# Performance work log

Hardware: AMD Instinct MI355X
Metric: run time of the kernel (lower is better)

The kernel has to match this reference:

```python
import jax, jax.numpy as jnp
import numpy as np

N_TRAIN = 2000
N_ATOMS = 30
DIM_D = N_ATOMS * (N_ATOMS - 1) // 2   # 435 pairwise descriptor entries
DIM_I = 3 * N_ATOMS                    # 90 Cartesian dofs
N_PERMS = 12
SIG = 10.0

_ROWS, _COLS = np.tril_indices(N_ATOMS, -1)
_DR = np.arange(DIM_D)


def d_desc_from_comp(Rd):
    # Rd: [n, DIM_D, 3] compact pair derivatives -> full Jacobian [n, DIM_D, DIM_I]
    # each pair (a,b) contributes +d at atom a's 3 dofs and -d at atom b's.
    n = Rd.shape[0]
    out = jnp.zeros((n, DIM_D, N_ATOMS, 3), Rd.dtype)
    out = out.at[:, _DR, _ROWS, :].set(Rd)
    out = out.at[:, _DR, _COLS, :].set(-Rd)
    return out.reshape(n, DIM_D, DIM_I)


def setup_inputs() -> dict:
    key = jax.random.key(0)
    k1, k2 = jax.random.split(key)
    R_desc = jax.random.normal(k1, (N_TRAIN, DIM_D), jnp.float32)
    R_d_desc = jax.random.normal(k2, (N_TRAIN, DIM_D, 3), jnp.float32)
    # Build a permutation-consistent tril_perms_lin (identity + random atom perms).
    rng = np.random.RandomState(0)
    M = np.zeros((N_ATOMS, N_ATOMS), np.int64)
    M[_ROWS, _COLS] = np.arange(DIM_D)
    M[_COLS, _ROWS] = np.arange(DIM_D)
    tril_perms = np.empty((N_PERMS, DIM_D), np.int64)
    for p in range(N_PERMS):
        perm = np.arange(N_ATOMS) if p == 0 else rng.permutation(N_ATOMS)
        tril_perms[p] = M[perm[_ROWS], perm[_COLS]]
    tpl = (tril_perms + np.arange(N_PERMS)[:, None] * DIM_D).flatten(order='F')
    return {
        'R_desc': R_desc,
        'R_d_desc': R_d_desc,
        'tril_perms_lin': jnp.asarray(tpl),
        'j': 0,
    }


def reference(R_desc, R_d_desc, tril_perms_lin, j):
    q = np.sqrt(5.0) / SIG
    # column point j: expanded Jacobian [DIM_D, DIM_I]
    rj_d = d_desc_from_comp(R_d_desc[j][None])[0]
    # permutation-symmetrized descriptor / Jacobian for point j
    rj_desc_perms = jnp.tile(R_desc[j], N_PERMS)[tril_perms_lin].reshape(DIM_D, N_PERMS).T  # [P,D]
    rj_d_perms = jnp.tile(rj_d.T, (1, N_PERMS))[:, tril_perms_lin].reshape(DIM_I, DIM_D, N_PERMS)  # [3N,D,P]
    x_diffs = q * (R_desc[:, None, :] - rj_desc_perms[None])        # [n,P,D]
    x_dists = jnp.linalg.norm(x_diffs, axis=-1)                      # [n,P]
    exp_xs = jnp.exp(-x_dists) * (q * q / 3.0)                       # [n,P]
    exp_xs_1_x_dists = exp_xs * (1.0 + x_dists)                      # [n,P]
    # Matern-5/2 Hessian block assembly
    inner = jnp.einsum('npd,jdp->npj', x_diffs, rj_d_perms)          # [n,P,3N]
    diff_ab = jnp.einsum('npd,npj->ndj', x_diffs * exp_xs[:, :, None], inner)  # [n,D,3N]
    diff_ab = diff_ab - jnp.einsum('jdp,np->ndj', rj_d_perms, exp_xs_1_x_dists)
    Rd_full = d_desc_from_comp(R_d_desc)                             # [n,D,3N]
    k = jnp.einsum('ndj,ndk->nkj', diff_ab, Rd_full)                 # [n,3N,3N]
    return k.reshape(N_TRAIN * DIM_I, DIM_I)
```

## Files before the change

kernel.cpp:

```cpp
#include <hip/hip_runtime.h>
#include <math.h>

#define NA 30
#define ND 435
#define NI 90
#define NP 12
#define NNB (NA-1)
#define SST 91
#define NTHR 384

typedef float v2f __attribute__((ext_vector_type(2)));

struct Pre {
  int   pidx[NP][ND];
  int   sigma[NP][NA];
  int   sigma_inv[NP][NA];
  int   rowv[ND];
  int   colv[ND];
  float rjp[NP][ND];
  float spj[NA][SST];
  unsigned int gtab[NNB][NP][NA];
  alignas(16) unsigned int stab[NA][NA][NP];
  unsigned int hmask[NA][NA];
};

__device__ __forceinline__ int pair_index(int x, int y) {
  int hi = max(x, y), lo = min(x, y);
  return hi * (hi - 1) / 2 + lo;
}

__global__ void preA_kernel(const int* __restrict__ tpl, Pre* ws) {
  const int tid = threadIdx.x;
  const int nthr = blockDim.x;

  for (int d = tid; d < ND; d += nthr) {
    int a = (int)floorf((1.0f + sqrtf(1.0f + 8.0f * (float)d)) * 0.5f);
    while (a * (a - 1) / 2 > d) --a;
    while ((a + 1) * a / 2 <= d) ++a;
    ws->rowv[d] = a;
    ws->colv[d] = d - a * (a - 1) / 2;
  }
  for (int idx = tid; idx < NP * ND; idx += nthr) {
    int d = idx / NP, p = idx % NP;
    ws->pidx[p][d] = tpl[idx] - p * ND;
  }
  __syncthreads();
  for (int idx = tid; idx < NP * NA; idx += nthr) {
    int p = idx / NA, a = idx % NA;
    int u1 = (a == 0) ? 1 : 0;
    int u2 = (a <= 1) ? 2 : 1;
    int e1 = ws->pidx[p][pair_index(a, u1)];
    int e2 = ws->pidx[p][pair_index(a, u2)];
    int r1 = ws->rowv[e1], c1 = ws->colv[e1];
    int r2 = ws->rowv[e2], c2 = ws->colv[e2];
    int sa = (r1 == r2 || r1 == c2) ? r1 : c1;
    ws->sigma[p][a] = sa;
  }
  __syncthreads();
  for (int idx = tid; idx < NP * NA; idx += nthr) {
    int p = idx / NA, a = idx % NA;
    ws->sigma_inv[p][ws->sigma[p][a]] = a;
  }
  __syncthreads();
  for (int it = tid; it < NA * NA; it += nthr) {
    int a = it / NA, a2 = it % NA;
    unsigned m = 0;
#pragma unroll
    for (int p = 0; p < NP; ++p)
      if (ws->sigma[p][a] == a2) m |= (1u << p);
    ws->hmask[a][a2] = m;
  }
}

__global__ void preB_kernel(const float* __restrict__ R_desc,
                            const float* __restrict__ R_d_desc,
                            const int* __restrict__ jptr,
                            Pre* ws) {
  const int gid = blockIdx.x * blockDim.x + threadIdx.x;
  const int gsz = gridDim.x * blockDim.x;
  const int j = *jptr;

  for (int idx = gid; idx < NP * ND; idx += gsz) {
    int p = idx / ND, d = idx % ND;
    ws->rjp[p][d] = R_desc[(size_t)j * ND + ws->pidx[p][d]];
  }
  for (int idx = gid; idx < NA * SST; idx += gsz) {
    int a = idx / SST, r = idx % SST;
    float val = 0.f;
    if (r < NI) {
      int u = r / 3, c = r % 3;
      if (u != a) {
        int d = pair_index(a, u);
        float t = R_d_desc[(size_t)j * (ND * 3) + 3 * d + c];
        val = (a > u) ? t : -t;
      }
    }
    ((float*)ws->spj)[idx] = val;
  }
  for (int idx = gid; idx < NNB * NP * NA; idx += gsz) {
    int a = idx % NA;
    int r = idx / NA;
    int p = r % NP, k = r / NP;
    int u = k + (k >= a ? 1 : 0);
    int d = pair_index(a, u);
    int su = ws->sigma[p][u];
    ws->gtab[k][p][a] = (unsigned)d | ((unsigned)su << 9) | ((unsigned)u << 14);
  }
  for (int idx = gid; idx < NA * NA * NP; idx += gsz) {
    int p = idx % NP;
    int r = idx / NP;
    int a2 = r % NA, a = r / NA;
    unsigned int v = 0;
    if (ws->sigma[p][a] != a2) {
      int u = ws->sigma_inv[p][a2];
      int sa = ws->sigma[p][a];
      v = (unsigned)u | ((unsigned)sa << 5) | (1u << 15);
    }
    ws->stab[a][a2][p] = v;
  }
}

__global__ __launch_bounds__(NTHR, 4) void gdml_kernel(
    const float* __restrict__ R_desc,
    const float* __restrict__ R_d_desc,
    const Pre* __restrict__ ws,
    float* __restrict__ out) {
  const int n = blockIdx.x;
  const int tid = threadIdx.x;

  __shared__ float rn_l[ND];
  __shared__ float S[NA * SST];
  __shared__ float Sp[NA * SST];
  __shared__ float v_s[NP * NI];
  __shared__ float w_s[NP * NI];
  __shared__ alignas(16) unsigned short HhU[NA * NP * 9];
  __shared__ float dist2[NP];
  __shared__ float e_s[NP], e1_s[NP];

  const float q   = 0.22360679774997896f;
  const float qq3 = 0.016666666666666666f;

  if (tid < NP) dist2[tid] = 0.f;
  for (int d = tid; d < ND; d += NTHR) rn_l[d] = R_desc[(size_t)n * ND + d];
  float* raw = (float*)HhU;
  for (int i = tid; i < ND * 3; i += NTHR)
    raw[i] = R_d_desc[(size_t)n * (ND * 3) + i];
  for (int i = tid; i < NA * SST; i += NTHR)
    Sp[i] = ((const float*)ws->spj)[i];
  __syncthreads();

  for (int i = tid; i < NA * NI; i += NTHR) {
    int a = i / NI, r = i % NI;
    int u = r / 3, c = r % 3;
    float val = 0.f;
    if (u != a) {
      int d = pair_index(a, u);
      float t = raw[3 * d + c];
      val = (a > u) ? t : -t;
    }
    S[a * SST + r] = val;
  }
  __syncthreads();

  float h[9];
  const int a_i = tid % NA, p_i = tid / NA;
  const bool act = (tid < NP * NA);
  if (act) {
    int sa = ws->sigma[p_i][a_i];
    const float* Srow = S + a_i * SST;
    const float* Prow = Sp + sa * SST;
    const float* rjpp = &ws->rjp[p_i][0];
    v2f V01 = {0.f, 0.f}; float V2 = 0.f;
    v2f I01 = {0.f, 0.f}; float I2 = 0.f;
    v2f H0 = {0.f, 0.f}, H1 = {0.f, 0.f}, H2 = {0.f, 0.f};
    float Hc0 = 0.f, Hc1 = 0.f, Hc2 = 0.f;
    float xq = 0.f;
    for (int k = 0; k < NNB; ++k) {
      unsigned g = ws->gtab[k][p_i][a_i];
      int d  = g & 511;
      int su = (g >> 9) & 31;
      int u  = (g >> 14) & 31;
      float x = q * (rn_l[d] - rjpp[d]);
      xq += x * x;
      float s0 = Srow[3 * u], s1 = Srow[3 * u + 1], s2 = Srow[3 * u + 2];
      float t0 = Prow[3 * su], t1 = Prow[3 * su + 1], t2 = Prow[3 * su + 2];
      V01 += (v2f){x, x} * (v2f){s0, s1}; V2 += x * s2;
      I01 += (v2f){x, x} * (v2f){t0, t1}; I2 += x * t2;
      v2f t01 = {t0, t1};
      H0 += (v2f){s0, s0} * t01; Hc0 += s0 * t2;
      H1 += (v2f){s1, s1} * t01; Hc1 += s1 * t2;
      H2 += (v2f){s2, s2} * t01; Hc2 += s2 * t2;
    }
    v_s[p_i * NI + 3 * a_i + 0] = V01.x;
    v_s[p_i * NI + 3 * a_i + 1] = V01.y;
    v_s[p_i * NI + 3 * a_i + 2] = V2;
    w_s[p_i * NI + 3 * sa + 0] = I01.x;
    w_s[p_i * NI + 3 * sa + 1] = I01.y;
    w_s[p_i * NI + 3 * sa + 2] = I2;
    atomicAdd(&dist2[p_i], xq);
    h[0] = H0.x; h[1] = H0.y; h[2] = Hc0;
    h[3] = H1.x; h[4] = H1.y; h[5] = Hc1;
    h[6] = H2.x; h[7] = H2.y; h[8] = Hc2;
  }
  __syncthreads();

  if (tid < NP) {
    float dist = sqrtf(dist2[tid] * 0.5f);
    float e = expf(-dist) * qq3;
    e_s[tid] = e;
    e1_s[tid] = e * (1.f + dist);
  }
  if (act) {
    unsigned short* hb = &HhU[(a_i * NP + p_i) * 9];
#pragma unroll
    for (int r = 0; r < 9; ++r) {
      unsigned bi = __float_as_uint(h[r]);
      hb[r] = (unsigned short)((bi + 0x7FFFu + ((bi >> 16) & 1u)) >> 16);
    }
  }
  __syncthreads();

  for (int i = tid; i < NP * NI; i += NTHR) v_s[i] *= e_s[i / NI];
  __syncthreads();

  float e1r[NP];
#pragma unroll
  for (int p = 0; p < NP; ++p) e1r[p] = e1_s[p];

  float* outn = out + (size_t)n * (NI * NI);
  for (int it = tid; it < NA * NA; it += NTHR) {
    int a = it / NA, a2 = it % NA;
    const float* Srow = S + a * SST;
    v2f A0 = {0.f, 0.f}, A1 = {0.f, 0.f}, A2 = {0.f, 0.f};
    float B0 = 0.f, B1 = 0.f, B2 = 0.f;
    const uint4* st4 = (const uint4*)&ws->stab[a][a2][0];
    uint4 ua = st4[0], ub = st4[1], uc = st4[2];
    unsigned stv[12] = {ua.x, ua.y, ua.z, ua.w, ub.x, ub.y, ub.z, ub.w,
                        uc.x, uc.y, uc.z, uc.w};
#pragma unroll
    for (int p = 0; p < NP; ++p) {
      float v0 = v_s[p * NI + 3 * a + 0];
      float v1 = v_s[p * NI + 3 * a + 1];
      float v2v = v_s[p * NI + 3 * a + 2];
      float w0 = w_s[p * NI + 3 * a2 + 0];
      float w1 = w_s[p * NI + 3 * a2 + 1];
      float w2 = w_s[p * NI + 3 * a2 + 2];
      v2f w01 = {w0, w1};
      A0 += (v2f){v0, v0} * w01;   B0 += v0 * w2;
      A1 += (v2f){v1, v1} * w01;   B1 += v1 * w2;
      A2 += (v2f){v2v, v2v} * w01; B2 += v2v * w2;
      unsigned g = stv[p];
      float f = (g & (1u << 15)) ? e1r[p] : 0.f;
      int u  = g & 31;
      int sa = (g >> 5) & 31;
      float r0 = f * Srow[3 * u];
      float r1 = f * Srow[3 * u + 1];
      float r2 = f * Srow[3 * u + 2];
      float j0 = Sp[sa * SST + 3 * a2 + 0];
      float j1 = Sp[sa * SST + 3 * a2 + 1];
      float j2 = Sp[sa * SST + 3 * a2 + 2];
      v2f j01 = {j0, j1};
      A0 += (v2f){r0, r0} * j01; B0 += r0 * j2;
      A1 += (v2f){r1, r1} * j01; B1 += r1 * j2;
      A2 += (v2f){r2, r2} * j01; B2 += r2 * j2;
    }
    unsigned m = ws->hmask[a][a2];
    while (m) {
      int p = __ffs(m) - 1;
      m &= m - 1;
      float e1 = e1r[p];
      const unsigned short* hb = &HhU[(a * NP + p) * 9];
      float hf[9];
#pragma unroll
      for (int r = 0; r < 9; ++r)
        hf[r] = __uint_as_float((unsigned)hb[r] << 16);
      A0 -= e1 * (v2f){hf[0], hf[1]}; B0 -= e1 * hf[2];
      A1 -= e1 * (v2f){hf[3], hf[4]}; B1 -= e1 * hf[5];
      A2 -= e1 * (v2f){hf[6], hf[7]}; B2 -= e1 * hf[8];
    }
    float* ob = outn + (size_t)(3 * a) * NI + 3 * a2;
    ob[0] = A0.x;          ob[1] = A0.y;          ob[2] = B0;
    ob[NI + 0] = A1.x;     ob[NI + 1] = A1.y;     ob[NI + 2] = B1;
    ob[2 * NI + 0] = A2.x; ob[2 * NI + 1] = A2.y; ob[2 * NI + 2] = B2;
  }
}

extern "C" void kernel_launch(void* const* d_in, const int* in_sizes, int n_in,
                              void* d_out, int out_size, void* d_ws, size_t ws_size,
                              hipStream_t stream) {
  const float* R_desc   = (const float*)d_in[0];
  const float* R_d_desc = (const float*)d_in[1];
  const int*   tpl      = (const int*)d_in[2];
  const int*   jptr     = (const int*)d_in[3];
  float* out = (float*)d_out;
  Pre* ws = (Pre*)d_ws;

  const int n_train = in_sizes[0] / ND;

  hipLaunchKernelGGL(preA_kernel, dim3(1), dim3(256), 0, stream, tpl, ws);
  hipLaunchKernelGGL(preB_kernel, dim3(48), dim3(256), 0, stream,
                     R_desc, R_d_desc, jptr, ws);
  hipLaunchKernelGGL(gdml_kernel, dim3(n_train), dim3(NTHR), 0, stream,
                     R_desc, R_d_desc, ws, out);
}
```

Before: 91.76 us.

## Precompute per-sample descriptor diffs in LDS and drop expanded Jacobian matrix

```diff
diff --git a/kernel.cpp b/kernel.cpp
--- a/kernel.cpp
+++ b/kernel.cpp
@@ -19,7 +19,6 @@
   int   colv[ND];
   float rjp[NP][ND];
   float spj[NA][SST];
-  unsigned int gtab[NNB][NP][NA];
   alignas(16) unsigned int stab[NA][NA][NP];
   unsigned int hmask[NA][NA];
 };
@@ -97,15 +96,6 @@
     }
     ((float*)ws->spj)[idx] = val;
   }
-  for (int idx = gid; idx < NNB * NP * NA; idx += gsz) {
-    int a = idx % NA;
-    int r = idx / NA;
-    int p = r % NP, k = r / NP;
-    int u = k + (k >= a ? 1 : 0);
-    int d = pair_index(a, u);
-    int su = ws->sigma[p][u];
-    ws->gtab[k][p][a] = (unsigned)d | ((unsigned)su << 9) | ((unsigned)u << 14);
-  }
   for (int idx = gid; idx < NA * NA * NP; idx += gsz) {
     int p = idx % NP;
     int r = idx / NP;
@@ -113,8 +103,10 @@
     unsigned int v = 0;
     if (ws->sigma[p][a] != a2) {
       int u = ws->sigma_inv[p][a2];
+      int d1 = pair_index(a, u);
       int sa = ws->sigma[p][a];
-      v = (unsigned)u | ((unsigned)sa << 5) | (1u << 15);
+      v = (unsigned)d1 | ((unsigned)sa << 9) | (1u << 15);
+      if (a > u) v |= (1u << 14);
     }
     ws->stab[a][a2][p] = v;
   }
@@ -128,12 +120,12 @@
   const int n = blockIdx.x;
   const int tid = threadIdx.x;
 
-  __shared__ float rn_l[ND];
-  __shared__ float S[NA * SST];
+  __shared__ float xd[NP * ND];
+  __shared__ float Rdn_l[ND * 3];
   __shared__ float Sp[NA * SST];
   __shared__ float v_s[NP * NI];
   __shared__ float w_s[NP * NI];
-  __shared__ alignas(16) unsigned short HhU[NA * NP * 9];
+  __shared__ unsigned short sig_l[NP * 32];
   __shared__ float dist2[NP];
   __shared__ float e_s[NP], e1_s[NP];
 
@@ -141,55 +133,65 @@
   const float qq3 = 0.016666666666666666f;
 
   if (tid < NP) dist2[tid] = 0.f;
-  for (int d = tid; d < ND; d += NTHR) rn_l[d] = R_desc[(size_t)n * ND + d];
-  float* raw = (float*)HhU;
   for (int i = tid; i < ND * 3; i += NTHR)
-    raw[i] = R_d_desc[(size_t)n * (ND * 3) + i];
+    Rdn_l[i] = R_d_desc[(size_t)n * (ND * 3) + i];
   for (int i = tid; i < NA * SST; i += NTHR)
     Sp[i] = ((const float*)ws->spj)[i];
-  __syncthreads();
-
-  for (int i = tid; i < NA * NI; i += NTHR) {
-    int a = i / NI, r = i % NI;
-    int u = r / 3, c = r % 3;
-    float val = 0.f;
-    if (u != a) {
-      int d = pair_index(a, u);
-      float t = raw[3 * d + c];
-      val = (a > u) ? t : -t;
-    }
-    S[a * SST + r] = val;
-  }
-  __syncthreads();
+  if (tid < NP * NA) {
+    int p = tid / NA, a = tid % NA;
+    sig_l[p * 32 + a] = (unsigned short)ws->sigma[p][a];
+  }
+
+  float acc[NP];
+#pragma unroll
+  for (int p = 0; p < NP; ++p) acc[p] = 0.f;
+  for (int d = tid; d < ND; d += NTHR) {
+    float rn = R_desc[(size_t)n * ND + d];
+#pragma unroll
+    for (int p = 0; p < NP; ++p) {
+      float x = q * (rn - ws->rjp[p][d]);
+      xd[p * ND + d] = x;
+      acc[p] += x * x;
+    }
+  }
+#pragma unroll
+  for (int p = 0; p < NP; ++p) {
+    for (int off = 32; off; off >>= 1) acc[p] += __shfl_xor(acc[p], off);
+  }
+  __syncthreads();
+  if ((tid & 63) == 0) {
+#pragma unroll
+    for (int p = 0; p < NP; ++p) atomicAdd(&dist2[p], acc[p]);
+  }
 
   float h[9];
   const int a_i = tid % NA, p_i = tid / NA;
   const bool act = (tid < NP * NA);
   if (act) {
-    int sa = ws->sigma[p_i][a_i];
-    const float* Srow = S + a_i * SST;
-    const float* Prow = Sp + sa * SST;
-    const float* rjpp = &ws->rjp[p_i][0];
+    int sa = sig_l[p_i * 32 + a_i];
+    const float* xp = xd + p_i * ND;
+    const float* Pr = Sp + sa * SST;
     v2f V01 = {0.f, 0.f}; float V2 = 0.f;
     v2f I01 = {0.f, 0.f}; float I2 = 0.f;
     v2f H0 = {0.f, 0.f}, H1 = {0.f, 0.f}, H2 = {0.f, 0.f};
     float Hc0 = 0.f, Hc1 = 0.f, Hc2 = 0.f;
-    float xq = 0.f;
     for (int k = 0; k < NNB; ++k) {
-      unsigned g = ws->gtab[k][p_i][a_i];
-      int d  = g & 511;
-      int su = (g >> 9) & 31;
-      int u  = (g >> 14) & 31;
-      float x = q * (rn_l[d] - rjpp[d]);
-      xq += x * x;
-      float s0 = Srow[3 * u], s1 = Srow[3 * u + 1], s2 = Srow[3 * u + 2];
-      float t0 = Prow[3 * su], t1 = Prow[3 * su + 1], t2 = Prow[3 * su + 2];
-      V01 += (v2f){x, x} * (v2f){s0, s1}; V2 += x * s2;
-      I01 += (v2f){x, x} * (v2f){t0, t1}; I2 += x * t2;
+      int u = k + (k >= a_i ? 1 : 0);
+      int su = sig_l[p_i * 32 + u];
+      int hi = max(a_i, u), lo = min(a_i, u);
+      int d = (hi * (hi - 1) >> 1) + lo;
+      float x = xp[d];
+      float m = (a_i > u) ? 1.f : -1.f;
+      float n0 = Rdn_l[3 * d], n1 = Rdn_l[3 * d + 1], n2 = Rdn_l[3 * d + 2];
+      float t0 = Pr[3 * su], t1 = Pr[3 * su + 1], t2 = Pr[3 * su + 2];
+      float sx = m * x;
+      float sn0 = m * n0, sn1 = m * n1, sn2 = m * n2;
+      V01 += (v2f){sx, sx} * (v2f){n0, n1}; V2 += sx * n2;
+      I01 += (v2f){x, x} * (v2f){t0, t1};   I2 += x * t2;
       v2f t01 = {t0, t1};
-      H0 += (v2f){s0, s0} * t01; Hc0 += s0 * t2;
-      H1 += (v2f){s1, s1} * t01; Hc1 += s1 * t2;
-      H2 += (v2f){s2, s2} * t01; Hc2 += s2 * t2;
+      H0 += (v2f){sn0, sn0} * t01; Hc0 += sn0 * t2;
+      H1 += (v2f){sn1, sn1} * t01; Hc1 += sn1 * t2;
+      H2 += (v2f){sn2, sn2} * t01; Hc2 += sn2 * t2;
     }
     v_s[p_i * NI + 3 * a_i + 0] = V01.x;
     v_s[p_i * NI + 3 * a_i + 1] = V01.y;
@@ -197,7 +199,6 @@
     w_s[p_i * NI + 3 * sa + 0] = I01.x;
     w_s[p_i * NI + 3 * sa + 1] = I01.y;
     w_s[p_i * NI + 3 * sa + 2] = I2;
-    atomicAdd(&dist2[p_i], xq);
     h[0] = H0.x; h[1] = H0.y; h[2] = Hc0;
     h[3] = H1.x; h[4] = H1.y; h[5] = Hc1;
     h[6] = H2.x; h[7] = H2.y; h[8] = Hc2;
@@ -205,83 +206,111 @@
   __syncthreads();
 
   if (tid < NP) {
-    float dist = sqrtf(dist2[tid] * 0.5f);
+    float dist = sqrtf(dist2[tid]);
     float e = expf(-dist) * qq3;
     e_s[tid] = e;
     e1_s[tid] = e * (1.f + dist);
   }
+  float* Hh = xd;
   if (act) {
-    unsigned short* hb = &HhU[(a_i * NP + p_i) * 9];
-#pragma unroll
-    for (int r = 0; r < 9; ++r) {
-      unsigned bi = __float_as_uint(h[r]);
-      hb[r] = (unsigned short)((bi + 0x7FFFu + ((bi >> 16) & 1u)) >> 16);
-    }
-  }
-  __syncthreads();
-
-  for (int i = tid; i < NP * NI; i += NTHR) v_s[i] *= e_s[i / NI];
-  __syncthreads();
-
-  float e1r[NP];
-#pragma unroll
-  for (int p = 0; p < NP; ++p) e1r[p] = e1_s[p];
+    float* hb = &Hh[(a_i * NP + p_i) * 9];
+#pragma unroll
+    for (int r = 0; r < 9; ++r) hb[r] = h[r];
+  }
+  __syncthreads();
 
   float* outn = out + (size_t)n * (NI * NI);
-  for (int it = tid; it < NA * NA; it += NTHR) {
-    int a = it / NA, a2 = it % NA;
-    const float* Srow = S + a * SST;
-    v2f A0 = {0.f, 0.f}, A1 = {0.f, 0.f}, A2 = {0.f, 0.f};
-    float B0 = 0.f, B1 = 0.f, B2 = 0.f;
-    const uint4* st4 = (const uint4*)&ws->stab[a][a2][0];
-    uint4 ua = st4[0], ub = st4[1], uc = st4[2];
-    unsigned stv[12] = {ua.x, ua.y, ua.z, ua.w, ub.x, ub.y, ub.z, ub.w,
-                        uc.x, uc.y, uc.z, uc.w};
+  for (int qv = tid; qv < NA * 15; qv += NTHR) {
+    int a = qv / 15, c2 = qv % 15;
+    int a2x = c2, a2y = c2 + 15;
+    v2f AX0 = {0.f,0.f}, AX1 = {0.f,0.f}, AX2 = {0.f,0.f};
+    float BX0 = 0.f, BX1 = 0.f, BX2 = 0.f;
+    v2f AY0 = {0.f,0.f}, AY1 = {0.f,0.f}, AY2 = {0.f,0.f};
+    float BY0 = 0.f, BY1 = 0.f, BY2 = 0.f;
+    const uint4* sx4 = (const uint4*)&ws->stab[a][a2x][0];
+    const uint4* sy4 = (const uint4*)&ws->stab[a][a2y][0];
+    uint4 xa = sx4[0], xb = sx4[1], xc = sx4[2];
+    uint4 ya = sy4[0], yb = sy4[1], yc = sy4[2];
+    unsigned svx[12] = {xa.x, xa.y, xa.z, xa.w, xb.x, xb.y, xb.z, xb.w,
+                        xc.x, xc.y, xc.z, xc.w};
+    unsigned svy[12] = {ya.x, ya.y, ya.z, ya.w, yb.x, yb.y, yb.z, yb.w,
+                        yc.x, yc.y, yc.z, yc.w};
 #pragma unroll
     for (int p = 0; p < NP; ++p) {
-      float v0 = v_s[p * NI + 3 * a + 0];
-      float v1 = v_s[p * NI + 3 * a + 1];
-      float v2v = v_s[p * NI + 3 * a + 2];
-      float w0 = w_s[p * NI + 3 * a2 + 0];
-      float w1 = w_s[p * NI + 3 * a2 + 1];
-      float w2 = w_s[p * NI + 3 * a2 + 2];
-      v2f w01 = {w0, w1};
-      A0 += (v2f){v0, v0} * w01;   B0 += v0 * w2;
-      A1 += (v2f){v1, v1} * w01;   B1 += v1 * w2;
-      A2 += (v2f){v2v, v2v} * w01; B2 += v2v * w2;
-      unsigned g = stv[p];
-      float f = (g & (1u << 15)) ? e1r[p] : 0.f;
-      int u  = g & 31;
-      int sa = (g >> 5) & 31;
-      float r0 = f * Srow[3 * u];
-      float r1 = f * Srow[3 * u + 1];
-      float r2 = f * Srow[3 * u + 2];
-      float j0 = Sp[sa * SST + 3 * a2 + 0];
-      float j1 = Sp[sa * SST + 3 * a2 + 1];
-      float j2 = Sp[sa * SST + 3 * a2 + 2];
+      float e  = e_s[p];
+      float e1 = e1_s[p];
+      float v0 = e * v_s[p * NI + 3 * a + 0];
+      float v1 = e * v_s[p * NI + 3 * a + 1];
+      float v2v = e * v_s[p * NI + 3 * a + 2];
+      float wx0 = w_s[p * NI + 3 * a2x + 0];
+      float wx1 = w_s[p * NI + 3 * a2x + 1];
+      float wx2 = w_s[p * NI + 3 * a2x + 2];
+      float wy0 = w_s[p * NI + 3 * a2y + 0];
+      float wy1 = w_s[p * NI + 3 * a2y + 1];
+      float wy2 = w_s[p * NI + 3 * a2y + 2];
+      v2f wx01 = {wx0, wx1}, wy01 = {wy0, wy1};
+      AX0 += (v2f){v0, v0} * wx01;   BX0 += v0 * wx2;
+      AX1 += (v2f){v1, v1} * wx01;   BX1 += v1 * wx2;
+      AX2 += (v2f){v2v, v2v} * wx01; BX2 += v2v * wx2;
+      AY0 += (v2f){v0, v0} * wy01;   BY0 += v0 * wy2;
+      AY1 += (v2f){v1, v1} * wy01;   BY1 += v1 * wy2;
+      AY2 += (v2f){v2v, v2v} * wy01; BY2 += v2v * wy2;
+      unsigned g = svx[p];
+      float fs = (g & 0x8000u) ? ((g & 0x4000u) ? e1 : -e1) : 0.f;
+      int d1 = g & 511;
+      int sa = (g >> 9) & 31;
+      float r0 = fs * Rdn_l[3 * d1];
+      float r1 = fs * Rdn_l[3 * d1 + 1];
+      float r2 = fs * Rdn_l[3 * d1 + 2];
+      float j0 = Sp[sa * SST + 3 * a2x + 0];
+      float j1 = Sp[sa * SST + 3 * a2x + 1];
+      float j2 = Sp[sa * SST + 3 * a2x + 2];
       v2f j01 = {j0, j1};
-      A0 += (v2f){r0, r0} * j01; B0 += r0 * j2;
-      A1 += (v2f){r1, r1} * j01; B1 += r1 * j2;
-      A2 += (v2f){r2, r2} * j01; B2 += r2 * j2;
-    }
-    unsigned m = ws->hmask[a][a2];
+      AX0 += (v2f){r0, r0} * j01; BX0 += r0 * j2;
+      AX1 += (v2f){r1, r1} * j01; BX1 += r1 * j2;
+      AX2 += (v2f){r2, r2} * j01; BX2 += r2 * j2;
+      g = svy[p];
+      fs = (g & 0x8000u) ? ((g & 0x4000u) ? e1 : -e1) : 0.f;
+      d1 = g & 511;
+      sa = (g >> 9) & 31;
+      r0 = fs * Rdn_l[3 * d1];
+      r1 = fs * Rdn_l[3 * d1 + 1];
+      r2 = fs * Rdn_l[3 * d1 + 2];
+      j0 = Sp[sa * SST + 3 * a2y + 0];
+      j1 = Sp[sa * SST + 3 * a2y + 1];
+      j2 = Sp[sa * SST + 3 * a2y + 2];
+      j01 = (v2f){j0, j1};
+      AY0 += (v2f){r0, r0} * j01; BY0 += r0 * j2;
+      AY1 += (v2f){r1, r1} * j01; BY1 += r1 * j2;
+      AY2 += (v2f){r2, r2} * j01; BY2 += r2 * j2;
+    }
+    unsigned m = ws->hmask[a][a2x];
     while (m) {
       int p = __ffs(m) - 1;
       m &= m - 1;
-      float e1 = e1r[p];
-      const unsigned short* hb = &HhU[(a * NP + p) * 9];
-      float hf[9];
-#pragma unroll
-      for (int r = 0; r < 9; ++r)
-        hf[r] = __uint_as_float((unsigned)hb[r] << 16);
-      A0 -= e1 * (v2f){hf[0], hf[1]}; B0 -= e1 * hf[2];
-      A1 -= e1 * (v2f){hf[3], hf[4]}; B1 -= e1 * hf[5];
-      A2 -= e1 * (v2f){hf[6], hf[7]}; B2 -= e1 * hf[8];
-    }
-    float* ob = outn + (size_t)(3 * a) * NI + 3 * a2;
-    ob[0] = A0.x;          ob[1] = A0.y;          ob[2] = B0;
-    ob[NI + 0] = A1.x;     ob[NI + 1] = A1.y;     ob[NI + 2] = B1;
-    ob[2 * NI + 0] = A2.x; ob[2 * NI + 1] = A2.y; ob[2 * NI + 2] = B2;
+      float e1 = e1_s[p];
+      const float* hb = &Hh[(a * NP + p) * 9];
+      AX0 -= e1 * (v2f){hb[0], hb[1]}; BX0 -= e1 * hb[2];
+      AX1 -= e1 * (v2f){hb[3], hb[4]}; BX1 -= e1 * hb[5];
+      AX2 -= e1 * (v2f){hb[6], hb[7]}; BX2 -= e1 * hb[8];
+    }
+    m = ws->hmask[a][a2y];
+    while (m) {
+      int p = __ffs(m) - 1;
+      m &= m - 1;
+      float e1 = e1_s[p];
+      const float* hb = &Hh[(a * NP + p) * 9];
+      AY0 -= e1 * (v2f){hb[0], hb[1]}; BY0 -= e1 * hb[2];
+      AY1 -= e1 * (v2f){hb[3], hb[4]}; BY1 -= e1 * hb[5];
+      AY2 -= e1 * (v2f){hb[6], hb[7]}; BY2 -= e1 * hb[8];
+    }
+    float* ob = outn + (size_t)(3 * a) * NI + 3 * a2x;
+    ob[0] = AX0.x;  ob[1] = AX0.y;  ob[2] = BX0;
+    ob[45] = AY0.x; ob[46] = AY0.y; ob[47] = BY0;
+    ob[NI + 0] = AX1.x;  ob[NI + 1] = AX1.y;  ob[NI + 2] = BX1;
+    ob[NI + 45] = AY1.x; ob[NI + 46] = AY1.y; ob[NI + 47] = BY1;
+    ob[2 * NI + 0] = AX2.x;  ob[2 * NI + 1] = AX2.y;  ob[2 * NI + 2] = BX2;
+    ob[2 * NI + 45] = AY2.x; ob[2 * NI + 46] = AY2.y; ob[2 * NI + 47] = BY2;
   }
 }
 
```

Result: slower. 324.0 us (+253.1%).
